# Optimization experiments

Measured on AMD Instinct MI355X. Metric: run time of the kernel, lower is better.

## Reference

```python
import jax, jax.numpy as jnp
import numpy as np

D_MODEL = 1024
N_HEADS = 16
D_HEAD = D_MODEL // N_HEADS
D_FF = 4096
B, T = 2, 2048


def layer_norm(x, gamma, beta, eps=1e-5):
    mu = jnp.mean(x, axis=-1, keepdims=True)
    var = jnp.var(x, axis=-1, keepdims=True)
    return (x - mu) * jax.lax.rsqrt(var + eps) * gamma + beta


def setup_inputs() -> dict:
    key = jax.random.key(0)
    ks = jax.random.split(key, 8)
    s = D_MODEL ** -0.5
    return {
        "x": jax.random.normal(ks[0], (B, T, D_MODEL), dtype=jnp.float32),
        "w_qkv": jax.random.normal(ks[1], (D_MODEL, 3 * D_MODEL), dtype=jnp.float32) * s,
        "w_out": jax.random.normal(ks[2], (D_MODEL, D_MODEL), dtype=jnp.float32) * s,
        "ln1_g": jnp.ones((D_MODEL,), jnp.float32),
        "ln1_b": jnp.zeros((D_MODEL,), jnp.float32),
        "ln2_g": jnp.ones((D_MODEL,), jnp.float32),
        "ln2_b": jnp.zeros((D_MODEL,), jnp.float32),
        "w1": jax.random.normal(ks[3], (D_MODEL, D_FF), dtype=jnp.float32) * s,
        "b1": jnp.zeros((D_FF,), jnp.float32),
        "w2": jax.random.normal(ks[4], (D_FF, D_MODEL), dtype=jnp.float32) * (D_FF ** -0.5),
        "b2": jnp.zeros((D_MODEL,), jnp.float32),
    }


def reference(x, w_qkv, w_out, ln1_g, ln1_b, ln2_g, ln2_b, w1, b1, w2, b2):
    Bb, Tt, C = x.shape
    h = layer_norm(x, ln1_g, ln1_b)
    qkv = h @ w_qkv  # [B,T,3C]
    q, k, v = jnp.split(qkv, 3, axis=-1)

    def heads(t):  # [B,T,C] -> [B,H,T,Dh]
        return t.reshape(Bb, Tt, N_HEADS, D_HEAD).transpose(0, 2, 1, 3)

    q, k, v = heads(q), heads(k), heads(v)
    scale = D_HEAD ** -0.5
    attn = jnp.einsum("bhqd,bhkd->bhqk", q, k) * scale
    causal = jnp.tril(jnp.ones((Tt, Tt), dtype=bool))
    attn = jnp.where(causal[None, None], attn, -jnp.inf)
    attn = jax.nn.softmax(attn, axis=-1)
    out = jnp.einsum("bhqk,bhkd->bhqd", attn, v)
    out = out.transpose(0, 2, 1, 3).reshape(Bb, Tt, C)
    x = x + out @ w_out
    h2 = layer_norm(x, ln2_g, ln2_b)
    ff = jax.nn.gelu(h2 @ w1 + b1, approximate=False) @ w2 + b2
    return x + ff
```

## Files before the change

kernel.cpp:

```cpp
#include <hip/hip_runtime.h>
#include <hip/hip_bf16.h>
#include <cstdint>

#define DM 1024
#define DFF 4096
#define NB 2
#define TT 2048
#define NH 16
#define DH 64

typedef unsigned short u16;
typedef __bf16 bf16x8 __attribute__((ext_vector_type(8)));
typedef float f32x4 __attribute__((ext_vector_type(4)));

__device__ __forceinline__ u16 f2b(float f) {
    union { float f; unsigned u; } v; v.f = f;
    unsigned u = v.u;
    return (u16)((u + 0x7FFFu + ((u >> 16) & 1u)) >> 16);
}

__device__ __forceinline__ unsigned cvtpk(float a, float b) {
    unsigned r;
    asm("v_cvt_pk_bf16_f32 %0, %1, %2" : "=v"(r) : "v"(a), "v"(b));
    return r;
}

__device__ __forceinline__ f32x4 mfma_bf16(bf16x8 a, bf16x8 b, f32x4 c) {
    return __builtin_amdgcn_mfma_f32_16x16x32_bf16(a, b, c, 0, 0, 0);
}

__device__ __forceinline__ void gload_lds16(const void* g, void* l) {
    __builtin_amdgcn_global_load_lds((const __attribute__((address_space(1))) unsigned int*)g,
                                     (__attribute__((address_space(3))) unsigned int*)l, 16, 0, 0);
}

__global__ __launch_bounds__(256) void transW(const float* __restrict__ W, u16* __restrict__ Wt,
                                              int K, int N) {
    __shared__ float t[32][33];
    int tx = threadIdx.x & 31, ty = threadIdx.x >> 5;
    int k0 = blockIdx.y * 32, n0 = blockIdx.x * 32;
#pragma unroll
    for (int j = 0; j < 4; ++j)
        t[ty + 8 * j][tx] = W[(size_t)(k0 + ty + 8 * j) * N + n0 + tx];
    __syncthreads();
#pragma unroll
    for (int j = 0; j < 4; ++j)
        Wt[(size_t)(n0 + ty + 8 * j) * K + k0 + tx] = f2b(t[tx][ty + 8 * j]);
}

__global__ __launch_bounds__(256) void ln_kernel(const float* __restrict__ X,
                                                 const float* __restrict__ g,
                                                 const float* __restrict__ bt,
                                                 u16* __restrict__ H) {
    int row = blockIdx.x, tid = threadIdx.x;
    float4 v = ((const float4*)(X + (size_t)row * DM))[tid];
    float s = v.x + v.y + v.z + v.w;
    float ss = v.x * v.x + v.y * v.y + v.z * v.z + v.w * v.w;
#pragma unroll
    for (int off = 32; off >= 1; off >>= 1) {
        s += __shfl_xor(s, off);
        ss += __shfl_xor(ss, off);
    }
    __shared__ float sb[8];
    int w = tid >> 6, lane = tid & 63;
    if (lane == 0) { sb[w] = s; sb[4 + w] = ss; }
    __syncthreads();
    s = sb[0] + sb[1] + sb[2] + sb[3];
    ss = sb[4] + sb[5] + sb[6] + sb[7];
    float mu = s * (1.0f / DM);
    float var = ss * (1.0f / DM) - mu * mu;
    float rstd = rsqrtf(var + 1e-5f);
    float4 gv = ((const float4*)g)[tid];
    float4 bv = ((const float4*)bt)[tid];
    ushort4 hv;
    hv.x = f2b((v.x - mu) * rstd * gv.x + bv.x);
    hv.y = f2b((v.y - mu) * rstd * gv.y + bv.y);
    hv.z = f2b((v.z - mu) * rstd * gv.z + bv.z);
    hv.w = f2b((v.w - mu) * rstd * gv.w + bv.w);
    ((ushort4*)(H + (size_t)row * DM))[tid] = hv;
}

template <int MODE, int DBUF>
__global__ __launch_bounds__(256) void gemm_kernel(
    const u16* __restrict__ A, const u16* __restrict__ Bt, int M, int N, int K,
    u16* __restrict__ oq, u16* __restrict__ ok, u16* __restrict__ vt,
    const float* __restrict__ resid, float* __restrict__ outf,
    const float* __restrict__ bias, u16* __restrict__ outbf) {
    __shared__ __align__(16) u16 Alds[DBUF + 1][128][64];
    __shared__ __align__(16) u16 Blds[DBUF + 1][128][64];
    const int tid = threadIdx.x;
    const int lane = tid & 63;
    const int w = tid >> 6;
    const int wr = w >> 1, wc = w & 1;
    int bid = blockIdx.x + gridDim.x * blockIdx.y;
    const int nwg = gridDim.x * gridDim.y;
    bid = (bid & 7) * (nwg >> 3) + (bid >> 3);
    const int bm = (bid / gridDim.x) * 128, bn = (bid % gridDim.x) * 128;
    const int l15 = lane & 15, lg = lane >> 4;
    const int srow = tid >> 3, pch = tid & 7;
    const int lc = pch ^ (srow & 7);

    f32x4 acc[4][4] = {};
    const u16* Ap = A + (size_t)(bm + srow) * K + lc * 8;
    const u16* Bp = Bt + (size_t)(bn + srow) * K + lc * 8;

#define STAGE(buf, k0)                                                          \
    {                                                                           \
        _Pragma("unroll") for (int i = 0; i < 4; ++i) {                         \
            gload_lds16(Ap + (size_t)(32 * i) * K + (k0), &Alds[buf][srow + 32 * i][pch * 8]); \
            gload_lds16(Bp + (size_t)(32 * i) * K + (k0), &Blds[buf][srow + 32 * i][pch * 8]); \
        }                                                                       \
    }

#define COMPUTE(buf)                                                            \
    {                                                                           \
        _Pragma("unroll") for (int kk = 0; kk < 2; ++kk) {                      \
            bf16x8 af[4], bfr[4];                                               \
            _Pragma("unroll") for (int f = 0; f < 4; ++f) {                     \
                const int ar = wr * 64 + f * 16 + l15;                          \
                const int br = wc * 64 + f * 16 + l15;                          \
                const int kch = kk * 4 + lg;                                    \
                af[f] = *(const bf16x8*)&Alds[buf][ar][(kch ^ (ar & 7)) * 8];   \
                bfr[f] = *(const bf16x8*)&Blds[buf][br][(kch ^ (br & 7)) * 8];  \
            }                                                                   \
            _Pragma("unroll") for (int mi = 0; mi < 4; ++mi)                    \
                _Pragma("unroll") for (int ni = 0; ni < 4; ++ni)                \
                    acc[mi][ni] = mfma_bf16(af[mi], bfr[ni], acc[mi][ni]);      \
        }                                                                       \
    }

    if constexpr (DBUF == 0) {
        for (int k0 = 0; k0 < K; k0 += 64) {
            STAGE(0, k0);
            __syncthreads();
            COMPUTE(0);
            __syncthreads();
        }
    } else {
        STAGE(0, 0);
        for (int k0 = 0; k0 < K; k0 += 64) {
            const int cur = (k0 >> 6) & 1;
            if (k0 + 64 < K) {
                STAGE(cur ^ 1, k0 + 64);
                asm volatile("s_waitcnt vmcnt(8)" ::: "memory");
            } else {
                asm volatile("s_waitcnt vmcnt(0)" ::: "memory");
            }
            __builtin_amdgcn_sched_barrier(0);
            __builtin_amdgcn_s_barrier();
            __builtin_amdgcn_sched_barrier(0);
            COMPUTE(cur);
            __builtin_amdgcn_s_barrier();
        }
    }
#undef STAGE
#undef COMPUTE

    const int m0 = bm + wr * 64, n0 = bn + wc * 64;
#pragma unroll
    for (int mi = 0; mi < 4; ++mi) {
#pragma unroll
        for (int ni = 0; ni < 4; ++ni) {
            if constexpr (MODE == 0) {
                const int n = n0 + ni * 16 + l15;
                const int which = n >> 10;
                const int hh = (n >> 6) & 15, d = n & 63;
                const int mbase = m0 + mi * 16 + 4 * lg;
                const int bb = mbase >> 11, t = mbase & 2047;
                if (which == 2) {
                    ushort4 pv;
                    pv.x = f2b(acc[mi][ni][0]);
                    pv.y = f2b(acc[mi][ni][1]);
                    pv.z = f2b(acc[mi][ni][2]);
                    pv.w = f2b(acc[mi][ni][3]);
                    *(ushort4*)(vt + (((size_t)(bb * NH + hh)) * DH + d) * TT + t) = pv;
                } else {
                    u16* dst = which == 0 ? oq : ok;
                    const float sc = which == 0 ? 0.18033688f : 1.0f;
#pragma unroll
                    for (int r = 0; r < 4; ++r)
                        dst[(((size_t)(bb * NH + hh)) * TT + t + r) * DH + d] =
                            f2b(acc[mi][ni][r] * sc);
                }
            } else {
#pragma unroll
                for (int r = 0; r < 4; ++r) {
                    int m = m0 + mi * 16 + 4 * lg + r;
                    int n = n0 + ni * 16 + l15;
                    float v = acc[mi][ni][r];
                    if constexpr (MODE == 1) {
                        size_t o = (size_t)m * N + n;
                        outf[o] = resid[o] + v;
                    } else if constexpr (MODE == 2) {
                        float z = v + bias[n];
                        outbf[(size_t)m * N + n] =
                            f2b(0.5f * z * (1.0f + erff(z * 0.70710678118654752f)));
                    } else {
                        size_t o = (size_t)m * N + n;
                        outf[o] = resid[o] + v + bias[n];
                    }
                }
            }
        }
    }
}

__global__ __launch_bounds__(256) void attn_kernel(const u16* __restrict__ Q,
                                                   const u16* __restrict__ Kg,
                                                   const u16* __restrict__ Vtg,
                                                   u16* __restrict__ O) {
    __shared__ __align__(16) u16 Klds[2][64][64];
    __shared__ __align__(16) u16 Vlds[2][64][64];
    const int tid = threadIdx.x, lane = tid & 63, w = tid >> 6;
    const int l15 = lane & 15, lg = lane >> 4;

    int id = blockIdx.x + (blockIdx.y << 4);
    int sw = (id & 7) * 64 + (id >> 3);
    const int p = sw & 15, bh = sw >> 4;
    const size_t base = (size_t)bh * TT * DH;
    const int b = bh >> 4, hh = bh & 15;

    const int srow = tid >> 3, pch = tid & 7;
    const int lc = pch ^ (srow & 7);

    const int src0 = (((2 * lg) & 3) << 4) | l15;
    const int src1 = src0 + 16;
    const bool hi = (lg >> 1) != 0;

#define ASTAGE(buf, kv)                                                                     \
    {                                                                                       \
        gload_lds16(Kg + base + (size_t)((kv) * 64 + srow) * DH + lc * 8,                   \
                    &Klds[buf][srow][pch * 8]);                                             \
        gload_lds16(Kg + base + (size_t)((kv) * 64 + srow + 32) * DH + lc * 8,              \
                    &Klds[buf][srow + 32][pch * 8]);                                        \
        gload_lds16(Vtg + base + (size_t)srow * TT + (kv) * 64 + lc * 8,                    \
                    &Vlds[buf][srow][pch * 8]);                                             \
        gload_lds16(Vtg + base + (size_t)(srow + 32) * TT + (kv) * 64 + lc * 8,             \
                    &Vlds[buf][srow + 32][pch * 8]);                                        \
    }

    for (int half = 0; half < 2; ++half) {
        const int qt = half ? (31 - p) : p;
        const int nkv = qt + 1;
        const int qrow = qt * 64 + w * 16 + l15;
        uint4 qu0 = *(const uint4*)(Q + base + (size_t)qrow * DH + 8 * lg);
        uint4 qu1 = *(const uint4*)(Q + base + (size_t)qrow * DH + 32 + 8 * lg);
        asm volatile("" : "+v"(qu0.x), "+v"(qu0.y), "+v"(qu0.z), "+v"(qu0.w),
                          "+v"(qu1.x), "+v"(qu1.y), "+v"(qu1.z), "+v"(qu1.w));
        const bf16x8 qf0 = *(const bf16x8*)&qu0;
        const bf16x8 qf1 = *(const bf16x8*)&qu1;

        ASTAGE(0, 0);

        f32x4 o[4] = {};
        float mrun = -INFINITY, lsum = 0.0f;

        int cur = 0;
        for (int kv = 0; kv < nkv; ++kv) {
            if (kv + 1 < nkv) {
                ASTAGE(cur ^ 1, kv + 1);
                asm volatile("s_waitcnt vmcnt(4)" ::: "memory");
            } else {
                asm volatile("s_waitcnt vmcnt(0)" ::: "memory");
            }
            __builtin_amdgcn_sched_barrier(0);
            __builtin_amdgcn_s_barrier();
            __builtin_amdgcn_sched_barrier(0);

            f32x4 s[4] = {};
#pragma unroll
            for (int nf = 0; nf < 4; ++nf) {
                const int row = nf * 16 + l15;
                bf16x8 kb0 = *(const bf16x8*)&Klds[cur][row][(lg ^ (l15 & 7)) * 8];
                bf16x8 kb1 = *(const bf16x8*)&Klds[cur][row][((4 + lg) ^ (l15 & 7)) * 8];
                s[nf] = mfma_bf16(kb0, qf0, s[nf]);
                s[nf] = mfma_bf16(kb1, qf1, s[nf]);
            }

            if (kv == qt) {
#pragma unroll
                for (int nf = 0; nf < 4; ++nf) {
                    const int tg = kv * 64 + nf * 16 + 4 * lg;
#pragma unroll
                    for (int r = 0; r < 4; ++r)
                        if (tg + r > qrow) s[nf][r] = -1e30f;
                }
            }

            f32x4 m4 = s[0];
#pragma unroll
            for (int nf = 1; nf < 4; ++nf) {
                m4[0] = fmaxf(m4[0], s[nf][0]);
                m4[1] = fmaxf(m4[1], s[nf][1]);
                m4[2] = fmaxf(m4[2], s[nf][2]);
                m4[3] = fmaxf(m4[3], s[nf][3]);
            }
            float pmax = fmaxf(fmaxf(m4[0], m4[1]), fmaxf(m4[2], m4[3]));
            pmax = fmaxf(pmax, __shfl_xor(pmax, 16));
            pmax = fmaxf(pmax, __shfl_xor(pmax, 32));
            const float mnew = fmaxf(mrun, pmax);
            const float alpha = exp2f(mrun - mnew);
            mrun = mnew;
            float ps = 0.0f;
#pragma unroll
            for (int nf = 0; nf < 4; ++nf) {
#pragma unroll
                for (int r = 0; r < 4; ++r) {
                    const float pp = exp2f(s[nf][r] - mnew);
                    s[nf][r] = pp;
                    ps += pp;
                }
                o[nf] = o[nf] * alpha;
            }
            lsum = lsum * alpha + ps;

            unsigned pk[4][2];
#pragma unroll
            for (int nf = 0; nf < 4; ++nf) {
                pk[nf][0] = cvtpk(s[nf][0], s[nf][1]);
                pk[nf][1] = cvtpk(s[nf][2], s[nf][3]);
            }
            bf16x8 pa[2];
#pragma unroll
            for (int kf = 0; kf < 2; ++kf) {
                unsigned a0 = __shfl((int)pk[2 * kf][0], src0);
                unsigned a1 = __shfl((int)pk[2 * kf][1], src0);
                unsigned a2 = __shfl((int)pk[2 * kf][0], src1);
                unsigned a3 = __shfl((int)pk[2 * kf][1], src1);
                unsigned c0 = __shfl((int)pk[2 * kf + 1][0], src0);
                unsigned c1 = __shfl((int)pk[2 * kf + 1][1], src0);
                unsigned c2 = __shfl((int)pk[2 * kf + 1][0], src1);
                unsigned c3 = __shfl((int)pk[2 * kf + 1][1], src1);
                uint4 wv;
                wv.x = hi ? c0 : a0;
                wv.y = hi ? c1 : a1;
                wv.z = hi ? c2 : a2;
                wv.w = hi ? c3 : a3;
                pa[kf] = *(const bf16x8*)&wv;
            }

#pragma unroll
            for (int nf = 0; nf < 4; ++nf) {
                const int row = nf * 16 + l15;
                bf16x8 vb0 = *(const bf16x8*)&Vlds[cur][row][(lg ^ (l15 & 7)) * 8];
                bf16x8 vb1 = *(const bf16x8*)&Vlds[cur][row][((4 + lg) ^ (l15 & 7)) * 8];
                o[nf] = mfma_bf16(vb0, pa[0], o[nf]);
                o[nf] = mfma_bf16(vb1, pa[1], o[nf]);
            }

            __builtin_amdgcn_s_barrier();
            cur ^= 1;
        }

        lsum += __shfl_xor(lsum, 16);
        lsum += __shfl_xor(lsum, 32);
        const float linv = 1.0f / lsum;
#pragma unroll
        for (int nf = 0; nf < 4; ++nf) {
            ushort4 pv;
            pv.x = f2b(o[nf][0] * linv);
            pv.y = f2b(o[nf][1] * linv);
            pv.z = f2b(o[nf][2] * linv);
            pv.w = f2b(o[nf][3] * linv);
            *(ushort4*)(O + ((size_t)b * TT + qrow) * DM + hh * DH + nf * 16 + 4 * lg) = pv;
        }
    }
#undef ASTAGE
}

extern "C" void kernel_launch(void* const* d_in, const int* in_sizes, int n_in,
                              void* d_out, int out_size, void* d_ws, size_t ws_size,
                              hipStream_t stream) {
    const float* x = (const float*)d_in[0];
    const float* wqkv = (const float*)d_in[1];
    const float* wout = (const float*)d_in[2];
    const float* ln1g = (const float*)d_in[3];
    const float* ln1b = (const float*)d_in[4];
    const float* ln2g = (const float*)d_in[5];
    const float* ln2b = (const float*)d_in[6];
    const float* w1 = (const float*)d_in[7];
    const float* b1 = (const float*)d_in[8];
    const float* w2 = (const float*)d_in[9];
    const float* b2 = (const float*)d_in[10];
    float* out = (float*)d_out;
    char* ws = (char*)d_ws;

    u16* wqkv_t = (u16*)(ws + 0);
    u16* wout_t = (u16*)(ws + 6291456);
    u16* w1_t   = (u16*)(ws + 8388608);
    u16* w2_t   = (u16*)(ws + 16777216);
    u16* h_bf   = (u16*)(ws + 25165824);
    u16* q_bf   = (u16*)(ws + 33554432);
    u16* k_bf   = (u16*)(ws + 41943040);
    u16* vt_bf  = (u16*)(ws + 50331648);
    u16* at_bf  = (u16*)(ws + 58720256);
    float* x1   = (float*)(ws + 67108864);
    u16* ff1_bf = q_bf;

    transW<<<dim3(96, 32), 256, 0, stream>>>(wqkv, wqkv_t, 1024, 3072);
    transW<<<dim3(32, 32), 256, 0, stream>>>(wout, wout_t, 1024, 1024);
    transW<<<dim3(128, 32), 256, 0, stream>>>(w1, w1_t, 1024, 4096);
    transW<<<dim3(32, 128), 256, 0, stream>>>(w2, w2_t, 4096, 1024);

    ln_kernel<<<4096, 256, 0, stream>>>(x, ln1g, ln1b, h_bf);

    gemm_kernel<0, 0><<<dim3(24, 32), 256, 0, stream>>>(h_bf, wqkv_t, 4096, 3072, 1024,
                                                        q_bf, k_bf, vt_bf,
                                                        nullptr, nullptr, nullptr, nullptr);

    attn_kernel<<<dim3(16, 32), 256, 0, stream>>>(q_bf, k_bf, vt_bf, at_bf);

    gemm_kernel<1, 1><<<dim3(8, 32), 256, 0, stream>>>(at_bf, wout_t, 4096, 1024, 1024,
                                                       nullptr, nullptr, nullptr,
                                                       x, x1, nullptr, nullptr);

    ln_kernel<<<4096, 256, 0, stream>>>(x1, ln2g, ln2b, h_bf);

    gemm_kernel<2, 0><<<dim3(32, 32), 256, 0, stream>>>(h_bf, w1_t, 4096, 4096, 1024,
                                                        nullptr, nullptr, nullptr,
                                                        nullptr, nullptr, b1, ff1_bf);

    gemm_kernel<3, 1><<<dim3(8, 32), 256, 0, stream>>>(ff1_bf, w2_t, 4096, 1024, 4096,
                                                       nullptr, nullptr, nullptr,
                                                       x1, out, b2, nullptr);
}
```

Baseline: 270.3 us.

## Use fast tanh-form GELU, packed bf16 converts, MFMA priority, and double-buffered GEMMs

Replaces the erf-based GELU in the FF1 epilogue with a sigmoid/exp2 approximation (the tanh-style GELU form) that uses a hardware reciprocal. Replaces software bf16 rounding with the packed v_cvt_pk_bf16_f32 instruction across layernorm, QKV, and attention epilogues. Raises wave priority around the MFMA blocks in attention, and switches the QKV and FF1 GEMMs to the double-buffered LDS variant. The approximate GELU changes numerics relative to exact erf, and double buffering increases LDS use, which may lower occupancy.

```diff
diff --git a/kernel.cpp b/kernel.cpp
--- a/kernel.cpp
+++ b/kernel.cpp
@@ -23,6 +23,14 @@
     unsigned r;
     asm("v_cvt_pk_bf16_f32 %0, %1, %2" : "=v"(r) : "v"(a), "v"(b));
     return r;
+}
+
+__device__ __forceinline__ float gelu_fast(float z) {
+    const float u = z * z;
+    const float w = z * __builtin_fmaf(u, 0.10294324f, 2.3022082f);
+    const float e = exp2f(w);
+    const float r = __builtin_amdgcn_rcpf(1.0f + e);
+    return z - z * r;
 }
 
 __device__ __forceinline__ f32x4 mfma_bf16(bf16x8 a, bf16x8 b, f32x4 c) {
@@ -72,12 +80,10 @@
     float rstd = rsqrtf(var + 1e-5f);
     float4 gv = ((const float4*)g)[tid];
     float4 bv = ((const float4*)bt)[tid];
-    ushort4 hv;
-    hv.x = f2b((v.x - mu) * rstd * gv.x + bv.x);
-    hv.y = f2b((v.y - mu) * rstd * gv.y + bv.y);
-    hv.z = f2b((v.z - mu) * rstd * gv.z + bv.z);
-    hv.w = f2b((v.w - mu) * rstd * gv.w + bv.w);
-    ((ushort4*)(H + (size_t)row * DM))[tid] = hv;
+    uint2 hv;
+    hv.x = cvtpk((v.x - mu) * rstd * gv.x + bv.x, (v.y - mu) * rstd * gv.y + bv.y);
+    hv.y = cvtpk((v.z - mu) * rstd * gv.z + bv.z, (v.w - mu) * rstd * gv.w + bv.w);
+    ((uint2*)(H + (size_t)row * DM))[tid] = hv;
 }
 
 template <int MODE, int DBUF>
@@ -168,35 +174,45 @@
                 const int mbase = m0 + mi * 16 + 4 * lg;
                 const int bb = mbase >> 11, t = mbase & 2047;
                 if (which == 2) {
-                    ushort4 pv;
-                    pv.x = f2b(acc[mi][ni][0]);
-                    pv.y = f2b(acc[mi][ni][1]);
-                    pv.z = f2b(acc[mi][ni][2]);
-                    pv.w = f2b(acc[mi][ni][3]);
-                    *(ushort4*)(vt + (((size_t)(bb * NH + hh)) * DH + d) * TT + t) = pv;
+                    uint2 pv;
+                    pv.x = cvtpk(acc[mi][ni][0], acc[mi][ni][1]);
+                    pv.y = cvtpk(acc[mi][ni][2], acc[mi][ni][3]);
+                    *(uint2*)(vt + (((size_t)(bb * NH + hh)) * DH + d) * TT + t) = pv;
                 } else {
                     u16* dst = which == 0 ? oq : ok;
                     const float sc = which == 0 ? 0.18033688f : 1.0f;
-#pragma unroll
-                    for (int r = 0; r < 4; ++r)
-                        dst[(((size_t)(bb * NH + hh)) * TT + t + r) * DH + d] =
-                            f2b(acc[mi][ni][r] * sc);
+                    const unsigned p01 = cvtpk(acc[mi][ni][0] * sc, acc[mi][ni][1] * sc);
+                    const unsigned p23 = cvtpk(acc[mi][ni][2] * sc, acc[mi][ni][3] * sc);
+                    u16* db = dst + (((size_t)(bb * NH + hh)) * TT + t) * DH + d;
+                    db[0] = (u16)p01;
+                    db[DH] = (u16)(p01 >> 16);
+                    db[2 * DH] = (u16)p23;
+                    db[3 * DH] = (u16)(p23 >> 16);
                 }
+            } else if constexpr (MODE == 2) {
+                const int n = n0 + ni * 16 + l15;
+                const float bn_ = bias[n];
+                const float g0 = gelu_fast(acc[mi][ni][0] + bn_);
+                const float g1 = gelu_fast(acc[mi][ni][1] + bn_);
+                const float g2 = gelu_fast(acc[mi][ni][2] + bn_);
+                const float g3 = gelu_fast(acc[mi][ni][3] + bn_);
+                const unsigned p01 = cvtpk(g0, g1);
+                const unsigned p23 = cvtpk(g2, g3);
+                u16* db = outbf + (size_t)(m0 + mi * 16 + 4 * lg) * N + n;
+                db[0] = (u16)p01;
+                db[N] = (u16)(p01 >> 16);
+                db[2 * N] = (u16)p23;
+                db[3 * N] = (u16)(p23 >> 16);
             } else {
 #pragma unroll
                 for (int r = 0; r < 4; ++r) {
                     int m = m0 + mi * 16 + 4 * lg + r;
                     int n = n0 + ni * 16 + l15;
                     float v = acc[mi][ni][r];
+                    size_t o = (size_t)m * N + n;
                     if constexpr (MODE == 1) {
-                        size_t o = (size_t)m * N + n;
                         outf[o] = resid[o] + v;
-                    } else if constexpr (MODE == 2) {
-                        float z = v + bias[n];
-                        outbf[(size_t)m * N + n] =
-                            f2b(0.5f * z * (1.0f + erff(z * 0.70710678118654752f)));
                     } else {
-                        size_t o = (size_t)m * N + n;
                         outf[o] = resid[o] + v + bias[n];
                     }
                 }
@@ -268,6 +284,7 @@
             __builtin_amdgcn_sched_barrier(0);
 
             f32x4 s[4] = {};
+            __builtin_amdgcn_s_setprio(1);
 #pragma unroll
             for (int nf = 0; nf < 4; ++nf) {
                 const int row = nf * 16 + l15;
@@ -276,6 +293,7 @@
                 s[nf] = mfma_bf16(kb0, qf0, s[nf]);
                 s[nf] = mfma_bf16(kb1, qf1, s[nf]);
             }
+            __builtin_amdgcn_s_setprio(0);
 
             if (kv == qt) {
 #pragma unroll
@@ -339,6 +357,7 @@
                 pa[kf] = *(const bf16x8*)&wv;
             }
 
+            __builtin_amdgcn_s_setprio(1);
 #pragma unroll
             for (int nf = 0; nf < 4; ++nf) {
                 const int row = nf * 16 + l15;
@@ -347,6 +366,7 @@
                 o[nf] = mfma_bf16(vb0, pa[0], o[nf]);
                 o[nf] = mfma_bf16(vb1, pa[1], o[nf]);
             }
+            __builtin_amdgcn_s_setprio(0);
 
             __builtin_amdgcn_s_barrier();
             cur ^= 1;
@@ -357,12 +377,10 @@
         const float linv = 1.0f / lsum;
 #pragma unroll
         for (int nf = 0; nf < 4; ++nf) {
-            ushort4 pv;
-            pv.x = f2b(o[nf][0] * linv);
-            pv.y = f2b(o[nf][1] * linv);
-            pv.z = f2b(o[nf][2] * linv);
-            pv.w = f2b(o[nf][3] * linv);
-            *(ushort4*)(O + ((size_t)b * TT + qrow) * DM + hh * DH + nf * 16 + 4 * lg) = pv;
+            uint2 pv;
+            pv.x = cvtpk(o[nf][0] * linv, o[nf][1] * linv);
+            pv.y = cvtpk(o[nf][2] * linv, o[nf][3] * linv);
+            *(uint2*)(O + ((size_t)b * TT + qrow) * DM + hh * DH + nf * 16 + 4 * lg) = pv;
         }
     }
 #undef ASTAGE
@@ -404,7 +422,7 @@
 
     ln_kernel<<<4096, 256, 0, stream>>>(x, ln1g, ln1b, h_bf);
 
-    gemm_kernel<0, 0><<<dim3(24, 32), 256, 0, stream>>>(h_bf, wqkv_t, 4096, 3072, 1024,
+    gemm_kernel<0, 1><<<dim3(24, 32), 256, 0, stream>>>(h_bf, wqkv_t, 4096, 3072, 1024,
                                                         q_bf, k_bf, vt_bf,
                                                         nullptr, nullptr, nullptr, nullptr);
 
@@ -416,7 +434,7 @@
 
     ln_kernel<<<4096, 256, 0, stream>>>(x1, ln2g, ln2b, h_bf);
 
-    gemm_kernel<2, 0><<<dim3(32, 32), 256, 0, stream>>>(h_bf, w1_t, 4096, 4096, 1024,
+    gemm_kernel<2, 1><<<dim3(32, 32), 256, 0, stream>>>(h_bf, w1_t, 4096, 4096, 1024,
                                                         nullptr, nullptr, nullptr,
                                                         nullptr, nullptr, b1, ff1_bf);
 
```

Measured after the change: 262.7 us. 2.8% less time.
